# Kernel tuning notes

Measured on AMD Instinct MI355X. Metric: run time of the kernel, lower is better.

Reference implementation:

```python
import jax, jax.numpy as jnp
import numpy as np

L = 3
ALPHA = 1.0
BETA = 1.0
SCALING = 3.0
N_NODES = 100000
N_EDGES = 1250000
D_FEAT = 64


def spmm(row, col, w, z, n):
    # out[i] = sum_{e: row_e == i} w_e * z[col_e]  (torch_sparse.matmul reduce='sum')
    return jax.ops.segment_sum(z[col] * w[:, None], row, num_segments=n)


def setup_inputs() -> dict:
    key = jax.random.key(0)
    k1, k2, k3, k4 = jax.random.split(key, 4)
    x = jax.random.normal(k1, (N_NODES, D_FEAT), dtype=jnp.float32)
    edge_index = jax.random.randint(k2, (2, N_EDGES), 0, N_NODES, dtype=jnp.int64)
    # surrogate for symmetric-normalized adjacency weights
    edge_weight = jax.random.uniform(k3, (N_EDGES,), dtype=jnp.float32) * 0.2
    gammas = jnp.full((L + 1, 1), min(1.0 / SCALING, 1.0), dtype=jnp.float32)
    return {"x": x, "edge_index": edge_index, "edge_weight": edge_weight, "gammas": gammas}


def reference(x, edge_index, edge_weight, gammas):
    n = x.shape[0]
    row, col = edge_index[0], edge_index[1]
    a, b = ALPHA, BETA

    zs = [x]  # z_0 = x
    # l = 1: c * z0 + (a+b+2)/2 * A z0
    z1 = ((a - b) / 2) * zs[-1] + ((a + b + 2) / 2) * spmm(row, col, edge_weight, zs[-1], n)
    zs.append(z1)
    for l in range(2, L + 1):
        c0 = 2 * l * (l + a + b) * (2 * l + a + b - 2)
        c1 = (2 * l + a + b - 1) * (a ** 2 - b ** 2)
        c2 = (2 * l + a + b - 1) * (2 * l + a + b) * (2 * l + a + b - 2)
        c3 = 2 * (l + a - 1) * (l + b - 1) * (2 * l + a + b)
        Az = spmm(row, col, edge_weight, zs[-1], n)
        z = (c1 * zs[-1] + c2 * Az - c3 * zs[-2]) / c0
        zs.append(z)

    coefs = jnp.cumprod(jnp.tanh(gammas) * SCALING, axis=0)  # [L+1, 1]
    Z = jnp.stack(zs, axis=1)  # [N, L+1, d]
    return (Z * coefs).mean(axis=1)
```

## Files before the change

### kernel.cpp

```cpp
#include <hip/hip_runtime.h>
#include <hip/hip_fp16.h>
#include <math.h>

#define D 64
#define RB_SHIFT 6
#define RB 64
#define CAP 1024
#define CAPE 2048
#define MAX_NB 1600


__global__ void bin_scatter_kernel(const int* __restrict__ row, const int* __restrict__ col,
                                   const float* __restrict__ w,
                                   int* __restrict__ cursor,
                                   int2* __restrict__ binned, int E, int NB) {
    __shared__ int lbase[MAX_NB];
    __shared__ int lcur[MAX_NB];
    int chunk = (E + gridDim.x - 1) / gridDim.x;
    int lo = blockIdx.x * chunk;
    int hi = min(E, lo + chunk);
    for (int j = threadIdx.x; j < NB; j += blockDim.x) { lbase[j] = 0; lcur[j] = 0; }
    __syncthreads();
    for (int i = lo + threadIdx.x; i < hi; i += blockDim.x)
        atomicAdd(&lbase[row[i] >> RB_SHIFT], 1);
    __syncthreads();
    for (int j = threadIdx.x; j < NB; j += blockDim.x) {
        int c = lbase[j];
        int base = c ? atomicAdd(&cursor[j], c) : 0;
        lbase[j] = j * CAP + base;
    }
    __syncthreads();
    for (int i = lo + threadIdx.x; i < hi; i += blockDim.x) {
        int r = row[i];
        int b = r >> RB_SHIFT;
        int off = atomicAdd(&lcur[b], 1);
        binned[lbase[b] + off] = make_int2(col[i] | ((r & (RB - 1)) << 17), __float_as_int(w[i]));
    }
}

__global__ void bucket_sort_kernel(const int2* __restrict__ binned,
                                   const int* __restrict__ cursor,
                                   int2* __restrict__ edges, int2* __restrict__ rowinfo,
                                   int N, int NB) {
    __shared__ int2 perm[CAPE];
    __shared__ int hist[RB];
    __shared__ int plr[RB];
    __shared__ int scn[RB];
    __shared__ int pst[RB];
    __shared__ int cur[RB];
    int b = blockIdx.x, t = threadIdx.x;
    int base = b * CAP;
    int cnt = cursor[b];
    if (cnt > CAP) cnt = CAP;

    if (t < RB) hist[t] = 0;
    __syncthreads();
    for (int i = t; i < cnt; i += 256)
        atomicAdd(&hist[(binned[base + i].x >> 17) & (RB - 1)], 1);
    __syncthreads();
    if (t < RB) plr[t] = (hist[t] + 7) & ~7;
    __syncthreads();
    if (t < RB) scn[t] = max(plr[t], plr[t ^ 1]);
    __syncthreads();
    for (int off = 1; off < RB; off <<= 1) {
        int v = (t < RB && t >= off) ? scn[t - off] : 0;
        __syncthreads();
        if (t < RB) scn[t] += v;
        __syncthreads();
    }
    if (t < RB) {
        int pl = max(plr[t], plr[t ^ 1]);
        int ps = scn[t] - pl;
        pst[t] = ps;
        cur[t] = ps;
    }
    __syncthreads();
    for (int i = t; i < cnt; i += 256) {
        int2 e = binned[base + i];
        int rl = (e.x >> 17) & (RB - 1);
        int d = atomicAdd(&cur[rl], 1);
        __half2 wh2 = __half2half2(__float2half(__int_as_float(e.y)));
        perm[d] = make_int2((e.x & 0x1FFFF) << 7, *(int*)&wh2);
    }
    __syncthreads();
    if (t < RB) {
        int h = hist[t];
        int ps = pst[t];
        int pl = max(plr[t], plr[t ^ 1]);
        int dummycol = (h > 0) ? perm[ps].x : 0;
        for (int i = h; i < pl; ++i) perm[ps + i] = make_int2(dummycol, 0);
        int r0 = b * RB + t;
        if (r0 < N) rowinfo[r0] = make_int2(b * CAPE + ps, pl);
    }
    __syncthreads();
    int ptotal = scn[RB - 1];
    if (ptotal > CAPE) ptotal = CAPE;
    for (int i = t; i < ptotal; i += 256) edges[b * CAPE + i] = perm[i];
}

__global__ void tohalf_kernel(const float4* __restrict__ in, ushort4* __restrict__ o, int n4) {
    int i = blockIdx.x * blockDim.x + threadIdx.x;
    int stride = gridDim.x * blockDim.x;
    for (; i < n4; i += stride) {
        float4 f = in[i];
        ushort4 h;
        h.x = __half_as_ushort(__float2half(f.x));
        h.y = __half_as_ushort(__float2half(f.y));
        h.z = __half_as_ushort(__float2half(f.z));
        h.w = __half_as_ushort(__float2half(f.w));
        o[i] = h;
    }
}

__device__ __forceinline__ __half2 half_row_acc(const int2* __restrict__ ep, int cnt,
                                                const char* __restrict__ g2b, int koff) {
    __half2 acc = __half2half2(__ushort_as_half((unsigned short)0));
    for (int jb = 0; jb < cnt; jb += 8) {
        int2 dd[8];
#pragma unroll
        for (int q = 0; q < 8; ++q) dd[q] = ep[jb + q];
        __half2 v[8];
#pragma unroll
        for (int q = 0; q < 8; ++q)
            v[q] = *(const __half2*)(g2b + (size_t)(unsigned)(dd[q].x + koff));
#pragma unroll
        for (int q = 0; q < 8; ++q) {
            int wb = dd[q].y;
            acc = __hfma2(*(__half2*)&wb, v[q], acc);
        }
    }
    return acc;
}

__global__ void spmm_z_kernel(const int2* __restrict__ rowinfo,
                              const int2* __restrict__ edges,
                              const __half2* __restrict__ gsrc2,
                              const __half2* __restrict__ zp2_2,
                              __half2* __restrict__ zdst2,
                              float cA, float cC, int N) {
    int gid = blockIdx.x * blockDim.x + threadIdx.x;
    int wv = gid >> 6;
    int lane = threadIdx.x & 63;
    int half = lane >> 5;
    int k = lane & 31;
    int r = 2 * wv + half;
    if (2 * wv >= N) return;
    if (r >= N) r = N - 1;

    int2 ri = rowinfo[r];
    int cnt = __builtin_amdgcn_readfirstlane(ri.y);

    __half2 acc = half_row_acc(edges + ri.x, cnt, (const char*)gsrc2, k * 4);
    float2 a = __half22float2(acc);

    size_t idx2 = (size_t)r * 32 + k;
    float2 z = make_float2(cA * a.x, cA * a.y);
    if (zp2_2) {
        float2 p2 = __half22float2(zp2_2[idx2]);
        z.x = fmaf(cC, p2.x, z.x);
        z.y = fmaf(cC, p2.y, z.y);
    }
    zdst2[idx2] = __floats2half2_rn(z.x, z.y);
}

__global__ void spmm_final_kernel(const int2* __restrict__ rowinfo,
                                  const int2* __restrict__ edges,
                                  const __half2* __restrict__ z2h2,
                                  const __half2* __restrict__ z1h2,
                                  const __half2* __restrict__ xh2,
                                  float* __restrict__ out,
                                  const float* __restrict__ gammas,
                                  float cA, float cC, int N) {
    int gid = blockIdx.x * blockDim.x + threadIdx.x;
    int wv = gid >> 6;
    int lane = threadIdx.x & 63;
    int half = lane >> 5;
    int k = lane & 31;
    int r = 2 * wv + half;
    if (2 * wv >= N) return;
    if (r >= N) r = N - 1;

    float t0 = tanhf(gammas[0]) * 3.0f;
    float t1 = t0 * (tanhf(gammas[1]) * 3.0f);
    float t2 = t1 * (tanhf(gammas[2]) * 3.0f);
    float t3 = t2 * (tanhf(gammas[3]) * 3.0f);

    int2 ri = rowinfo[r];
    int cnt = __builtin_amdgcn_readfirstlane(ri.y);

    __half2 acc = half_row_acc(edges + ri.x, cnt, (const char*)z2h2, k * 4);
    float2 a = __half22float2(acc);

    size_t idx2 = (size_t)r * 32 + k;
    float2 z1v = __half22float2(z1h2[idx2]);
    float2 z2v = __half22float2(z2h2[idx2]);
    float2 xv  = __half22float2(xh2[idx2]);
    float2 z3 = make_float2(cA * a.x + cC * z1v.x, cA * a.y + cC * z1v.y);
    float2 o;
    o.x = 0.25f * (t0 * xv.x + t1 * z1v.x + t2 * z2v.x + t3 * z3.x);
    o.y = 0.25f * (t0 * xv.y + t1 * z1v.y + t2 * z2v.y + t3 * z3.y);
    ((float2*)out)[idx2] = o;
}

extern "C" void kernel_launch(void* const* d_in, const int* in_sizes, int n_in,
                              void* d_out, int out_size, void* d_ws, size_t ws_size,
                              hipStream_t stream) {
    const float* x      = (const float*)d_in[0];
    const int*   ei     = (const int*)d_in[1];
    const float* w      = (const float*)d_in[2];
    const float* gammas = (const float*)d_in[3];

    const int E = in_sizes[1] / 2;
    const int N = in_sizes[0] / D;
    const long NF = (long)N * D;
    const int NB = (N + RB - 1) >> RB_SHIFT;

    float* out = (float*)d_out;

    char* p = (char*)d_ws;
    __half* xh  = (__half*)p;       p += NF * sizeof(__half);
    __half* z1h = (__half*)p;       p += NF * sizeof(__half);
    __half* z2h = (__half*)p;       p += NF * sizeof(__half);
    int* cursor = (int*)p;          p += NB * sizeof(int);
    p = (char*)(((uintptr_t)p + 15) & ~(uintptr_t)15);
    int2* rowinfo = (int2*)p;       p += (size_t)N * sizeof(int2);
    int2* binned = (int2*)p;        p += (size_t)NB * CAP * sizeof(int2);
    int2* edges = (int2*)p;

    const int* row = ei;
    const int* col = ei + E;

    const double a = 1.0, b = 1.0;
    const int blk = 256;

    hipMemsetAsync(cursor, 0, (size_t)NB * sizeof(int), stream);
    bin_scatter_kernel<<<256, 1024, 0, stream>>>(row, col, w, cursor, binned, E, NB);
    bucket_sort_kernel<<<NB, 256, 0, stream>>>(binned, cursor, edges, rowinfo, N, NB);
    tohalf_kernel<<<1024, blk, 0, stream>>>((const float4*)x, (ushort4*)xh, (int)(NF / 4));

    const int nwaves = (N + 1) / 2;
    const int sgrid = (nwaves + 3) / 4;

    {
        float cA = (float)((a + b + 2.0) / 2.0);
        spmm_z_kernel<<<sgrid, blk, 0, stream>>>(rowinfo, edges, (const __half2*)xh,
                                                 nullptr, (__half2*)z1h, cA, 0.0f, N);
    }

    {
        int l = 2;
        double c0 = 2.0 * l * (l + a + b) * (2.0 * l + a + b - 2.0);
        double c2 = (2.0 * l + a + b - 1.0) * (2.0 * l + a + b) * (2.0 * l + a + b - 2.0);
        double c3 = 2.0 * (l + a - 1.0) * (l + b - 1.0) * (2.0 * l + a + b);
        spmm_z_kernel<<<sgrid, blk, 0, stream>>>(rowinfo, edges, (const __half2*)z1h,
                                                 (const __half2*)xh, (__half2*)z2h,
                                                 (float)(c2 / c0), (float)(-c3 / c0), N);
    }

    {
        int l = 3;
        double c0 = 2.0 * l * (l + a + b) * (2.0 * l + a + b - 2.0);
        double c2 = (2.0 * l + a + b - 1.0) * (2.0 * l + a + b) * (2.0 * l + a + b - 2.0);
        double c3 = 2.0 * (l + a - 1.0) * (l + b - 1.0) * (2.0 * l + a + b);
        spmm_final_kernel<<<sgrid, blk, 0, stream>>>(rowinfo, edges, (const __half2*)z2h,
                                                     (const __half2*)z1h, (const __half2*)xh,
                                                     out, gammas,
                                                     (float)(c2 / c0), (float)(-c3 / c0), N);
    }
}
```

Measured before the change: 206.6 us.

## Pair rows by sorted degree within buckets to balance half-wave work

Inside each 64-row bucket, rows are ranked by padded degree and paired with similar-degree neighbours, so the two rows sharing a wavefront have nearly equal edge counts and less padding. A new per-half-wave info table (start, padded length, row id) replaces the per-row table, and the edge loader uses 16-byte int4 loads to fetch two edges at once. The per-bucket edge capacity grows to 3072, which enlarges shared memory and the workspace. The O(RB^2) rank computation adds some setup cost to the sort kernel.

```diff
diff --git a/kernel.cpp b/kernel.cpp
--- a/kernel.cpp
+++ b/kernel.cpp
@@ -6,7 +6,7 @@
 #define RB_SHIFT 6
 #define RB 64
 #define CAP 1024
-#define CAPE 2048
+#define CAPE 3072
 #define MAX_NB 1600
 
 
@@ -40,14 +40,16 @@
 
 __global__ void bucket_sort_kernel(const int2* __restrict__ binned,
                                    const int* __restrict__ cursor,
-                                   int2* __restrict__ edges, int2* __restrict__ rowinfo,
+                                   int2* __restrict__ edges, int4* __restrict__ hwinfo,
                                    int N, int NB) {
     __shared__ int2 perm[CAPE];
     __shared__ int hist[RB];
-    __shared__ int plr[RB];
-    __shared__ int scn[RB];
-    __shared__ int pst[RB];
+    __shared__ int plen[RB];
+    __shared__ int srow[RB];
+    __shared__ int pclr[RB];
+    __shared__ int st[RB];
     __shared__ int cur[RB];
+    __shared__ int pb[RB / 2];
     int b = blockIdx.x, t = threadIdx.x;
     int base = b * CAP;
     int cnt = cursor[b];
@@ -58,22 +60,38 @@
     for (int i = t; i < cnt; i += 256)
         atomicAdd(&hist[(binned[base + i].x >> 17) & (RB - 1)], 1);
     __syncthreads();
-    if (t < RB) plr[t] = (hist[t] + 7) & ~7;
-    __syncthreads();
-    if (t < RB) scn[t] = max(plr[t], plr[t ^ 1]);
-    __syncthreads();
-    for (int off = 1; off < RB; off <<= 1) {
-        int v = (t < RB && t >= off) ? scn[t - off] : 0;
+    if (t < RB) plen[t] = (hist[t] + 7) & ~7;
+    __syncthreads();
+    if (t < RB) {
+        int len = plen[t], rk = 0;
+        for (int j = 0; j < RB; ++j) {
+            int lj = plen[j];
+            rk += (lj < len) || (lj == len && j < t);
+        }
+        srow[rk] = t;
+    }
+    __syncthreads();
+    if (t < RB / 2) pb[t] = 2 * max(plen[srow[2 * t]], plen[srow[2 * t + 1]]);
+    __syncthreads();
+    for (int off = 1; off < RB / 2; off <<= 1) {
+        int v = (t < RB / 2 && t >= off) ? pb[t - off] : 0;
         __syncthreads();
-        if (t < RB) scn[t] += v;
+        if (t < RB / 2) pb[t] += v;
         __syncthreads();
     }
-    if (t < RB) {
-        int pl = max(plr[t], plr[t ^ 1]);
-        int ps = scn[t] - pl;
-        pst[t] = ps;
-        cur[t] = ps;
-    }
+    if (t < RB / 2) {
+        int m = t;
+        int rA = srow[2 * m], rB2 = srow[2 * m + 1];
+        int pcl = max(plen[rA], plen[rB2]);
+        int baseP = pb[m] - 2 * pcl;
+        st[rA] = baseP;         pclr[rA] = pcl;
+        st[rB2] = baseP + pcl;  pclr[rB2] = pcl;
+        int gb = b * CAPE;
+        hwinfo[(size_t)b * RB + 2 * m]     = make_int4(gb + baseP, pcl, b * RB + rA, 0);
+        hwinfo[(size_t)b * RB + 2 * m + 1] = make_int4(gb + baseP + pcl, pcl, b * RB + rB2, 0);
+    }
+    __syncthreads();
+    if (t < RB) cur[t] = st[t];
     __syncthreads();
     for (int i = t; i < cnt; i += 256) {
         int2 e = binned[base + i];
@@ -85,15 +103,13 @@
     __syncthreads();
     if (t < RB) {
         int h = hist[t];
-        int ps = pst[t];
-        int pl = max(plr[t], plr[t ^ 1]);
+        int ps = st[t];
+        int pl = pclr[t];
         int dummycol = (h > 0) ? perm[ps].x : 0;
         for (int i = h; i < pl; ++i) perm[ps + i] = make_int2(dummycol, 0);
-        int r0 = b * RB + t;
-        if (r0 < N) rowinfo[r0] = make_int2(b * CAPE + ps, pl);
-    }
-    __syncthreads();
-    int ptotal = scn[RB - 1];
+    }
+    __syncthreads();
+    int ptotal = pb[RB / 2 - 1];
     if (ptotal > CAPE) ptotal = CAPE;
     for (int i = t; i < ptotal; i += 256) edges[b * CAPE + i] = perm[i];
 }
@@ -114,43 +130,48 @@
 
 __device__ __forceinline__ __half2 half_row_acc(const int2* __restrict__ ep, int cnt,
                                                 const char* __restrict__ g2b, int koff) {
+    const int4* ep4 = (const int4*)ep;
     __half2 acc = __half2half2(__ushort_as_half((unsigned short)0));
     for (int jb = 0; jb < cnt; jb += 8) {
-        int2 dd[8];
+        int4 dd[4];
 #pragma unroll
-        for (int q = 0; q < 8; ++q) dd[q] = ep[jb + q];
+        for (int q = 0; q < 4; ++q) dd[q] = ep4[(jb >> 1) + q];
         __half2 v[8];
 #pragma unroll
-        for (int q = 0; q < 8; ++q)
-            v[q] = *(const __half2*)(g2b + (size_t)(unsigned)(dd[q].x + koff));
+        for (int q = 0; q < 4; ++q) {
+            v[2 * q]     = *(const __half2*)(g2b + (size_t)(unsigned)(dd[q].x + koff));
+            v[2 * q + 1] = *(const __half2*)(g2b + (size_t)(unsigned)(dd[q].z + koff));
+        }
 #pragma unroll
-        for (int q = 0; q < 8; ++q) {
-            int wb = dd[q].y;
-            acc = __hfma2(*(__half2*)&wb, v[q], acc);
+        for (int q = 0; q < 4; ++q) {
+            int w0 = dd[q].y, w1 = dd[q].w;
+            acc = __hfma2(*(__half2*)&w0, v[2 * q], acc);
+            acc = __hfma2(*(__half2*)&w1, v[2 * q + 1], acc);
         }
     }
     return acc;
 }
 
-__global__ void spmm_z_kernel(const int2* __restrict__ rowinfo,
+__global__ void spmm_z_kernel(const int4* __restrict__ hwinfo,
                               const int2* __restrict__ edges,
                               const __half2* __restrict__ gsrc2,
                               const __half2* __restrict__ zp2_2,
                               __half2* __restrict__ zdst2,
-                              float cA, float cC, int N) {
+                              float cA, float cC, int N, int NHW) {
     int gid = blockIdx.x * blockDim.x + threadIdx.x;
     int wv = gid >> 6;
     int lane = threadIdx.x & 63;
     int half = lane >> 5;
     int k = lane & 31;
-    int r = 2 * wv + half;
-    if (2 * wv >= N) return;
-    if (r >= N) r = N - 1;
-
-    int2 ri = rowinfo[r];
-    int cnt = __builtin_amdgcn_readfirstlane(ri.y);
-
-    __half2 acc = half_row_acc(edges + ri.x, cnt, (const char*)gsrc2, k * 4);
+    int hw = 2 * wv + half;
+    if (hw >= NHW) return;
+
+    int4 hi = hwinfo[hw];
+    int cnt = __builtin_amdgcn_readfirstlane(hi.y);
+
+    __half2 acc = half_row_acc(edges + hi.x, cnt, (const char*)gsrc2, k * 4);
+    int r = hi.z;
+    if (r >= N) return;
     float2 a = __half22float2(acc);
 
     size_t idx2 = (size_t)r * 32 + k;
@@ -163,32 +184,33 @@
     zdst2[idx2] = __floats2half2_rn(z.x, z.y);
 }
 
-__global__ void spmm_final_kernel(const int2* __restrict__ rowinfo,
+__global__ void spmm_final_kernel(const int4* __restrict__ hwinfo,
                                   const int2* __restrict__ edges,
                                   const __half2* __restrict__ z2h2,
                                   const __half2* __restrict__ z1h2,
                                   const __half2* __restrict__ xh2,
                                   float* __restrict__ out,
                                   const float* __restrict__ gammas,
-                                  float cA, float cC, int N) {
+                                  float cA, float cC, int N, int NHW) {
     int gid = blockIdx.x * blockDim.x + threadIdx.x;
     int wv = gid >> 6;
     int lane = threadIdx.x & 63;
     int half = lane >> 5;
     int k = lane & 31;
-    int r = 2 * wv + half;
-    if (2 * wv >= N) return;
-    if (r >= N) r = N - 1;
+    int hw = 2 * wv + half;
+    if (hw >= NHW) return;
 
     float t0 = tanhf(gammas[0]) * 3.0f;
     float t1 = t0 * (tanhf(gammas[1]) * 3.0f);
     float t2 = t1 * (tanhf(gammas[2]) * 3.0f);
     float t3 = t2 * (tanhf(gammas[3]) * 3.0f);
 
-    int2 ri = rowinfo[r];
-    int cnt = __builtin_amdgcn_readfirstlane(ri.y);
-
-    __half2 acc = half_row_acc(edges + ri.x, cnt, (const char*)z2h2, k * 4);
+    int4 hi = hwinfo[hw];
+    int cnt = __builtin_amdgcn_readfirstlane(hi.y);
+
+    __half2 acc = half_row_acc(edges + hi.x, cnt, (const char*)z2h2, k * 4);
+    int r = hi.z;
+    if (r >= N) return;
     float2 a = __half22float2(acc);
 
     size_t idx2 = (size_t)r * 32 + k;
@@ -214,6 +236,7 @@
     const int N = in_sizes[0] / D;
     const long NF = (long)N * D;
     const int NB = (N + RB - 1) >> RB_SHIFT;
+    const int NHW = NB * RB;
 
     float* out = (float*)d_out;
 
@@ -223,7 +246,7 @@
     __half* z2h = (__half*)p;       p += NF * sizeof(__half);
     int* cursor = (int*)p;          p += NB * sizeof(int);
     p = (char*)(((uintptr_t)p + 15) & ~(uintptr_t)15);
-    int2* rowinfo = (int2*)p;       p += (size_t)N * sizeof(int2);
+    int4* hwinfo = (int4*)p;        p += (size_t)NHW * sizeof(int4);
     int2* binned = (int2*)p;        p += (size_t)NB * CAP * sizeof(int2);
     int2* edges = (int2*)p;
 
@@ -235,16 +258,16 @@
 
     hipMemsetAsync(cursor, 0, (size_t)NB * sizeof(int), stream);
     bin_scatter_kernel<<<256, 1024, 0, stream>>>(row, col, w, cursor, binned, E, NB);
-    bucket_sort_kernel<<<NB, 256, 0, stream>>>(binned, cursor, edges, rowinfo, N, NB);
+    bucket_sort_kernel<<<NB, 256, 0, stream>>>(binned, cursor, edges, hwinfo, N, NB);
     tohalf_kernel<<<1024, blk, 0, stream>>>((const float4*)x, (ushort4*)xh, (int)(NF / 4));
 
-    const int nwaves = (N + 1) / 2;
+    const int nwaves = NHW / 2;
     const int sgrid = (nwaves + 3) / 4;
 
     {
         float cA = (float)((a + b + 2.0) / 2.0);
-        spmm_z_kernel<<<sgrid, blk, 0, stream>>>(rowinfo, edges, (const __half2*)xh,
-                                                 nullptr, (__half2*)z1h, cA, 0.0f, N);
+        spmm_z_kernel<<<sgrid, blk, 0, stream>>>(hwinfo, edges, (const __half2*)xh,
+                                                 nullptr, (__half2*)z1h, cA, 0.0f, N, NHW);
     }
 
     {
@@ -252,9 +275,9 @@
         double c0 = 2.0 * l * (l + a + b) * (2.0 * l + a + b - 2.0);
         double c2 = (2.0 * l + a + b - 1.0) * (2.0 * l + a + b) * (2.0 * l + a + b - 2.0);
         double c3 = 2.0 * (l + a - 1.0) * (l + b - 1.0) * (2.0 * l + a + b);
-        spmm_z_kernel<<<sgrid, blk, 0, stream>>>(rowinfo, edges, (const __half2*)z1h,
+        spmm_z_kernel<<<sgrid, blk, 0, stream>>>(hwinfo, edges, (const __half2*)z1h,
                                                  (const __half2*)xh, (__half2*)z2h,
-                                                 (float)(c2 / c0), (float)(-c3 / c0), N);
+                                                 (float)(c2 / c0), (float)(-c3 / c0), N, NHW);
     }
 
     {
@@ -262,9 +285,9 @@
         double c0 = 2.0 * l * (l + a + b) * (2.0 * l + a + b - 2.0);
         double c2 = (2.0 * l + a + b - 1.0) * (2.0 * l + a + b) * (2.0 * l + a + b - 2.0);
         double c3 = 2.0 * (l + a - 1.0) * (l + b - 1.0) * (2.0 * l + a + b);
-        spmm_final_kernel<<<sgrid, blk, 0, stream>>>(rowinfo, edges, (const __half2*)z2h,
+        spmm_final_kernel<<<sgrid, blk, 0, stream>>>(hwinfo, edges, (const __half2*)z2h,
                                                      (const __half2*)z1h, (const __half2*)xh,
                                                      out, gammas,
-                                                     (float)(c2 / c0), (float)(-c3 / c0), N);
-    }
-}
+                                                     (float)(c2 / c0), (float)(-c3 / c0), N, NHW);
+    }
+}
```

After: 230.0 us. 1.11x slower.
